# Kernel optimization log

Hardware: AMD Instinct MI355X
Metric: run time of the kernel (lower is better)

## Reference

```python
import jax, jax.numpy as jnp
import numpy as np

N, E, IN_DIM, OUT_DIM, H = 50000, 800000, 128, 16, 8


def setup_inputs() -> dict:
    key = jax.random.key(0)
    ks = jax.random.split(key, 10)
    h = jax.random.normal(ks[0], (N, IN_DIM), dtype=jnp.float32)
    row = jnp.sort(jax.random.randint(ks[1], (E,), 0, N))
    col = jax.random.randint(ks[2], (E,), 0, N)
    s = 1.0 / np.sqrt(IN_DIM)
    Wq = jax.random.normal(ks[3], (IN_DIM, OUT_DIM * H), dtype=jnp.float32) * s
    Wk = jax.random.normal(ks[4], (IN_DIM, OUT_DIM * H), dtype=jnp.float32) * s
    Wv = jax.random.normal(ks[5], (IN_DIM, OUT_DIM * H), dtype=jnp.float32) * s
    bq = jnp.zeros((OUT_DIM * H,), jnp.float32)
    bk = jnp.zeros((OUT_DIM * H,), jnp.float32)
    bv = jnp.zeros((OUT_DIM * H,), jnp.float32)
    return {"h": h, "Wq": Wq, "bq": bq, "Wk": Wk, "bk": bk, "Wv": Wv, "bv": bv,
            "row": row, "col": col}


def reference(h, Wq, bq, Wk, bk, Wv, bv, row, col):
    n = h.shape[0]
    scaling = OUT_DIM ** (-0.5)
    # projections, reshaped (N, out_dim, heads) as in the torch module
    q = (h @ Wq + bq).reshape(n, OUT_DIM, H) * scaling
    k = (h @ Wk + bk).reshape(n, OUT_DIM, H)
    v = (h @ Wv + bv).reshape(n, OUT_DIM, H)
    # bsddmm: per-edge, per-head dot product  score[e,h] = <q[row[e],:,h], k[col[e],:,h]>
    s = jnp.einsum('edh,edh->eh', q[row], k[col])  # [E, H]
    # sparse row-wise softmax (over each destination node's neighbors)
    m = jax.ops.segment_max(s, row, num_segments=n)       # [N, H]
    p = jnp.exp(s - m[row])                               # [E, H]
    z = jax.ops.segment_sum(p, row, num_segments=n)       # [N, H]
    attn = p / z[row]                                     # [E, H]
    # bspmm: out[i,d,h] = sum_{e: row[e]=i} attn[e,h] * v[col[e],d,h]
    out = jax.ops.segment_sum(attn[:, None, :] * v[col], row, num_segments=n)
    return out.reshape(n, -1)
```

## Files before the change

### kernel.cpp

```cpp
#include <hip/hip_runtime.h>
#include <math.h>

typedef unsigned int uint32;
typedef short short8 __attribute__((ext_vector_type(8)));
typedef float f32x4 __attribute__((ext_vector_type(4)));

union frag_u { short8 s; uint32 u[4]; uint4 q; };


__device__ __forceinline__ uint32 pack_bf16(float lo, float hi) {
    uint32 a = __float_as_uint(lo);
    uint32 b = __float_as_uint(hi);
    a = (a + 0x7FFFu + ((a >> 16) & 1u)) >> 16;
    b = (b + 0x7FFFu + ((b >> 16) & 1u)) & 0xFFFF0000u;
    return a | b;
}
__device__ __forceinline__ unsigned short bf16r(float x) {
    uint32 u = __float_as_uint(x);
    return (unsigned short)((u + 0x7FFFu + ((u >> 16) & 1u)) >> 16);
}

__global__ __launch_bounds__(256) void transpose_W_kernel(
    const float* __restrict__ Wq, const float* __restrict__ Wk,
    const float* __restrict__ Wv, uint32* __restrict__ Wt)
{
    __shared__ unsigned short tile[128][129];
    const int m = blockIdx.x;
    const float* W = (m == 0) ? Wq : (m == 1) ? Wk : Wv;
    const int t = threadIdx.x;

    const float4* W4 = reinterpret_cast<const float4*>(W);
    #pragma unroll
    for (int i0 = 0; i0 < 16; ++i0) {
        int i = t + i0 * 256;
        int k = i >> 5, nq = i & 31;
        float4 v = W4[i];
        tile[nq * 4 + 0][k] = bf16r(v.x);
        tile[nq * 4 + 1][k] = bf16r(v.y);
        tile[nq * 4 + 2][k] = bf16r(v.z);
        tile[nq * 4 + 3][k] = bf16r(v.w);
    }
    __syncthreads();
    uint32* out = Wt + (size_t)m * 8192;
    #pragma unroll
    for (int i0 = 0; i0 < 32; ++i0) {
        int i = t + i0 * 256;
        int n = i >> 6, kp = i & 63;
        out[i] = (uint32)tile[n][kp * 2] | ((uint32)tile[n][kp * 2 + 1] << 16);
    }
}

__global__ __launch_bounds__(256) void proj_mfma_kernel(
    const float* __restrict__ h, const uint32* __restrict__ Wt,
    const float* __restrict__ bq, const float* __restrict__ bk,
    const float* __restrict__ bv,
    uint32* __restrict__ Qp, uint2* __restrict__ KV, int N)
{
    const int t = threadIdx.x;
    const int lane = t & 63;
    const int w = t >> 6;
    const int r = lane & 15, g = lane >> 4;
    const int nbase = blockIdx.x * 64;

    frag_u afr[4][4];
    const float4* h4 = reinterpret_cast<const float4*>(h);
    #pragma unroll
    for (int ng = 0; ng < 4; ++ng) {
        int arow = nbase + ng * 16 + r;
        bool av = arow < N;
        #pragma unroll
        for (int kb = 0; kb < 4; ++kb) {
            float4 x = make_float4(0.f,0.f,0.f,0.f), y = x;
            if (av) {
                size_t base = (size_t)arow * 32 + (kb * 4 + g) * 2;
                x = h4[base]; y = h4[base + 1];
            }
            afr[ng][kb].u[0] = pack_bf16(x.x, x.y);
            afr[ng][kb].u[1] = pack_bf16(x.z, x.w);
            afr[ng][kb].u[2] = pack_bf16(y.x, y.y);
            afr[ng][kb].u[3] = pack_bf16(y.z, y.w);
        }
    }

    const float SCALE_Q = 0.25f * 1.44269504f;
    const int c = w * 16 + r;
    uint32 kpk[4][4];

    #pragma unroll
    for (int mat = 0; mat < 3; ++mat) {
        const uint32* wb = Wt + mat * 8192;
        frag_u bfr[2][4];
        #pragma unroll
        for (int tti = 0; tti < 2; ++tti)
            #pragma unroll
            for (int kb = 0; kb < 4; ++kb)
                bfr[tti][kb].q = *reinterpret_cast<const uint4*>(
                    wb + ((w + 4 * tti) * 16 + r) * 64 + (kb * 4 + g) * 4);

        f32x4 acc[4][2];
        #pragma unroll
        for (int ng = 0; ng < 4; ++ng)
            #pragma unroll
            for (int tti = 0; tti < 2; ++tti)
                acc[ng][tti] = (f32x4){0.f, 0.f, 0.f, 0.f};

        #pragma unroll
        for (int ng = 0; ng < 4; ++ng)
            #pragma unroll
            for (int tti = 0; tti < 2; ++tti)
                #pragma unroll
                for (int kb = 0; kb < 4; ++kb)
                    acc[ng][tti] = __builtin_amdgcn_mfma_f32_16x16x32_bf16(
                        afr[ng][kb].s, bfr[tti][kb].s, acc[ng][tti], 0, 0, 0);

        const float* bias = (mat == 0) ? bq : (mat == 1) ? bk : bv;
        float blo = bias[c], bhi = bias[c + 64];
        #pragma unroll
        for (int ng = 0; ng < 4; ++ng) {
            #pragma unroll
            for (int reg = 0; reg < 4; ++reg) {
                int node = nbase + ng * 16 + g * 4 + reg;
                float lo = acc[ng][0][reg] + blo;
                float hi = acc[ng][1][reg] + bhi;
                if (mat == 0) {
                    if (node < N)
                        Qp[(size_t)node * 64 + c] = pack_bf16(lo * SCALE_Q, hi * SCALE_Q);
                } else if (mat == 1) {
                    kpk[ng][reg] = pack_bf16(lo, hi);
                } else {
                    if (node < N)
                        KV[(size_t)node * 64 + c] = make_uint2(kpk[ng][reg], pack_bf16(lo, hi));
                }
            }
        }
    }
}

__global__ void row_ptr_kernel(const int* __restrict__ row, int* __restrict__ rp,
                               int N, int E)
{
    int i = blockIdx.x * blockDim.x + threadIdx.x;
    if (i > N) return;
    int lo = 0, hi = E;
    while (lo < hi) {
        int mid = (lo + hi) >> 1;
        if (row[mid] < i) lo = mid + 1; else hi = mid;
    }
    rp[i] = lo;
}

__global__ __launch_bounds__(256) void edge_attn_kernel(
    const uint32* __restrict__ Qp, const uint2* __restrict__ KV,
    const int* __restrict__ rp, const int* __restrict__ col,
    float* __restrict__ out, int N)
{
    const int lane = threadIdx.x & 63;
    const int node = blockIdx.x * 4 + (threadIdx.x >> 6);
    if (node >= N) return;
    const int hh   = lane & 7;
    const int slot = lane >> 3;

    const int start = rp[node], end = rp[node + 1];
    float* outp = out + (size_t)node * 128;
    if (start >= end) { outp[lane] = 0.f; outp[lane + 64] = 0.f; return; }
    const int last = end - 1;

    float q[16];
    {
        const uint32* qrow = Qp + (size_t)node * 64;
        #pragma unroll
        for (int i = 0; i < 8; ++i) {
            uint32 u = qrow[hh + 8 * i];
            q[2 * i]     = __uint_as_float(u << 16);
            q[2 * i + 1] = __uint_as_float(u & 0xFFFF0000u);
        }
    }

    float z = 0.f;
    float acc[16];
    #pragma unroll
    for (int i = 0; i < 16; ++i) acc[i] = 0.f;

    uint2 bufA[8], bufB[8];
    #define LOADG(buf, c0) { \
        const uint2* kvr = KV + (size_t)(c0) * 64; \
        _Pragma("unroll") \
        for (int i = 0; i < 8; ++i) (buf)[i] = kvr[hh + 8 * i]; }
    #define PROC(buf, gb) { \
        float s = 0.f; \
        _Pragma("unroll") \
        for (int i = 0; i < 8; ++i) { \
            s = fmaf(q[2*i],   __uint_as_float((buf)[i].x << 16), s); \
            s = fmaf(q[2*i+1], __uint_as_float((buf)[i].x & 0xFFFF0000u), s); } \
        float p = ((gb) + slot < end) ? __builtin_amdgcn_exp2f(s) : 0.f; \
        z += p; \
        _Pragma("unroll") \
        for (int i = 0; i < 8; ++i) { \
            acc[i]     = fmaf(p, __uint_as_float((buf)[i].y << 16), acc[i]); \
            acc[8 + i] = fmaf(p, __uint_as_float((buf)[i].y & 0xFFFF0000u), acc[8 + i]); } }

    int cA = col[min(start + slot, last)];
    int cB = col[min(start + 8 + slot, last)];
    LOADG(bufA, cA);
    int gb = start;
    while (true) {
        LOADG(bufB, cB);
        cA = col[min(gb + 16 + slot, last)];
        PROC(bufA, gb);
        gb += 8;
        if (gb >= end) break;
        LOADG(bufA, cA);
        cB = col[min(gb + 16 + slot, last)];
        PROC(bufB, gb);
        gb += 8;
        if (gb >= end) break;
    }

    #pragma unroll
    for (int m = 8; m <= 32; m <<= 1) {
        z += __shfl_xor(z, m);
        #pragma unroll
        for (int i = 0; i < 16; ++i) acc[i] += __shfl_xor(acc[i], m);
    }

    const float rz = 1.0f / z;
    outp[lane]      = acc[slot] * rz;
    outp[lane + 64] = acc[8 + slot] * rz;
}

extern "C" void kernel_launch(void* const* d_in, const int* in_sizes, int n_in,
                              void* d_out, int out_size, void* d_ws, size_t ws_size,
                              hipStream_t stream)
{
    const float* h  = (const float*)d_in[0];
    const float* Wq = (const float*)d_in[1];
    const float* bq = (const float*)d_in[2];
    const float* Wk = (const float*)d_in[3];
    const float* bk = (const float*)d_in[4];
    const float* Wv = (const float*)d_in[5];
    const float* bv = (const float*)d_in[6];
    const int* row  = (const int*)d_in[7];
    const int* col  = (const int*)d_in[8];
    float* out = (float*)d_out;

    const int N = in_sizes[0] / 128;
    const int E = in_sizes[7];

    uint2*  KV = (uint2*)d_ws;
    uint32* Qp = (uint32*)(KV + (size_t)N * 64);
    uint32* Wt = Qp + (size_t)N * 64;
    int*    rp = (int*)(Wt + 3 * 8192);

    transpose_W_kernel<<<3, 256, 0, stream>>>(Wq, Wk, Wv, Wt);
    row_ptr_kernel<<<(N + 256) / 256, 256, 0, stream>>>(row, rp, N, E);
    proj_mfma_kernel<<<(N + 63) / 64, 256, 0, stream>>>(
        h, Wt, bq, bk, bv, Qp, KV, N);
    edge_attn_kernel<<<(N + 3) / 4, 256, 0, stream>>>(Qp, KV, rp, col, out, N);
}
```

Before: 111.0 us.

## Switch intermediates from bf16 to fp16 with packed dot2 and merge prep kernels

Q/K/V and the transposed weights are now stored as fp16, made with the hardware pkrtz convert instead of manual bf16 rounding. The projection uses the f16 MFMA, and the edge kernel computes scores with packed fdot2 instructions in place of unpack-plus-FMA pairs. The weight-transpose and row-pointer kernels are merged into one launch to save launch overhead. Risks are fp16 range limits and round-toward-zero conversion changing accuracy.

```diff
diff --git a/kernel.cpp b/kernel.cpp
--- a/kernel.cpp
+++ b/kernel.cpp
@@ -2,51 +2,65 @@
 #include <math.h>
 
 typedef unsigned int uint32;
-typedef short short8 __attribute__((ext_vector_type(8)));
+typedef _Float16 f16x8 __attribute__((ext_vector_type(8)));
+typedef _Float16 f16x2 __attribute__((ext_vector_type(2)));
 typedef float f32x4 __attribute__((ext_vector_type(4)));
 
-union frag_u { short8 s; uint32 u[4]; uint4 q; };
-
-
-__device__ __forceinline__ uint32 pack_bf16(float lo, float hi) {
-    uint32 a = __float_as_uint(lo);
-    uint32 b = __float_as_uint(hi);
-    a = (a + 0x7FFFu + ((a >> 16) & 1u)) >> 16;
-    b = (b + 0x7FFFu + ((b >> 16) & 1u)) & 0xFFFF0000u;
-    return a | b;
-}
-__device__ __forceinline__ unsigned short bf16r(float x) {
-    uint32 u = __float_as_uint(x);
-    return (unsigned short)((u + 0x7FFFu + ((u >> 16) & 1u)) >> 16);
-}
-
-__global__ __launch_bounds__(256) void transpose_W_kernel(
+union frag_u { f16x8 h; uint32 u[4]; uint4 q; };
+
+
+__device__ __forceinline__ uint32 pack_f16(float lo, float hi) {
+    auto r = __builtin_amdgcn_cvt_pkrtz(lo, hi);
+    return __builtin_bit_cast(uint32, r);
+}
+__device__ __forceinline__ float dot2acc(uint32 a, uint32 b, float c) {
+#if __has_builtin(__builtin_amdgcn_fdot2)
+    return __builtin_amdgcn_fdot2(__builtin_bit_cast(f16x2, a),
+                                  __builtin_bit_cast(f16x2, b), c, false);
+#else
+    f16x2 av = __builtin_bit_cast(f16x2, a), bv = __builtin_bit_cast(f16x2, b);
+    return fmaf((float)av[0], (float)bv[0], fmaf((float)av[1], (float)bv[1], c));
+#endif
+}
+
+__global__ __launch_bounds__(256) void prep_kernel(
     const float* __restrict__ Wq, const float* __restrict__ Wk,
-    const float* __restrict__ Wv, uint32* __restrict__ Wt)
-{
-    __shared__ unsigned short tile[128][129];
-    const int m = blockIdx.x;
-    const float* W = (m == 0) ? Wq : (m == 1) ? Wk : Wv;
+    const float* __restrict__ Wv, uint32* __restrict__ Wt,
+    const int* __restrict__ row, int* __restrict__ rp, int N, int E)
+{
     const int t = threadIdx.x;
-
-    const float4* W4 = reinterpret_cast<const float4*>(W);
-    #pragma unroll
-    for (int i0 = 0; i0 < 16; ++i0) {
-        int i = t + i0 * 256;
-        int k = i >> 5, nq = i & 31;
-        float4 v = W4[i];
-        tile[nq * 4 + 0][k] = bf16r(v.x);
-        tile[nq * 4 + 1][k] = bf16r(v.y);
-        tile[nq * 4 + 2][k] = bf16r(v.z);
-        tile[nq * 4 + 3][k] = bf16r(v.w);
-    }
-    __syncthreads();
-    uint32* out = Wt + (size_t)m * 8192;
-    #pragma unroll
-    for (int i0 = 0; i0 < 32; ++i0) {
-        int i = t + i0 * 256;
-        int n = i >> 6, kp = i & 63;
-        out[i] = (uint32)tile[n][kp * 2] | ((uint32)tile[n][kp * 2 + 1] << 16);
+    if (blockIdx.x < 3) {
+        __shared__ unsigned short tile[128][129];
+        const int m = blockIdx.x;
+        const float* W = (m == 0) ? Wq : (m == 1) ? Wk : Wv;
+        const float4* W4 = reinterpret_cast<const float4*>(W);
+        #pragma unroll
+        for (int i0 = 0; i0 < 16; ++i0) {
+            int i = t + i0 * 256;
+            int k = i >> 5, nq = i & 31;
+            float4 v = W4[i];
+            tile[nq * 4 + 0][k] = (unsigned short)(pack_f16(v.x, 0.f) & 0xFFFFu);
+            tile[nq * 4 + 1][k] = (unsigned short)(pack_f16(v.y, 0.f) & 0xFFFFu);
+            tile[nq * 4 + 2][k] = (unsigned short)(pack_f16(v.z, 0.f) & 0xFFFFu);
+            tile[nq * 4 + 3][k] = (unsigned short)(pack_f16(v.w, 0.f) & 0xFFFFu);
+        }
+        __syncthreads();
+        uint32* out = Wt + (size_t)m * 8192;
+        #pragma unroll
+        for (int i0 = 0; i0 < 32; ++i0) {
+            int i = t + i0 * 256;
+            int n = i >> 6, kp = i & 63;
+            out[i] = (uint32)tile[n][kp * 2] | ((uint32)tile[n][kp * 2 + 1] << 16);
+        }
+    } else {
+        int i = (blockIdx.x - 3) * 256 + t;
+        if (i > N) return;
+        int lo = 0, hi = E;
+        while (lo < hi) {
+            int mid = (lo + hi) >> 1;
+            if (row[mid] < i) lo = mid + 1; else hi = mid;
+        }
+        rp[i] = lo;
     }
 }
 
@@ -75,10 +89,10 @@
                 size_t base = (size_t)arow * 32 + (kb * 4 + g) * 2;
                 x = h4[base]; y = h4[base + 1];
             }
-            afr[ng][kb].u[0] = pack_bf16(x.x, x.y);
-            afr[ng][kb].u[1] = pack_bf16(x.z, x.w);
-            afr[ng][kb].u[2] = pack_bf16(y.x, y.y);
-            afr[ng][kb].u[3] = pack_bf16(y.z, y.w);
+            afr[ng][kb].u[0] = pack_f16(x.x, x.y);
+            afr[ng][kb].u[1] = pack_f16(x.z, x.w);
+            afr[ng][kb].u[2] = pack_f16(y.x, y.y);
+            afr[ng][kb].u[3] = pack_f16(y.z, y.w);
         }
     }
 
@@ -110,8 +124,8 @@
             for (int tti = 0; tti < 2; ++tti)
                 #pragma unroll
                 for (int kb = 0; kb < 4; ++kb)
-                    acc[ng][tti] = __builtin_amdgcn_mfma_f32_16x16x32_bf16(
-                        afr[ng][kb].s, bfr[tti][kb].s, acc[ng][tti], 0, 0, 0);
+                    acc[ng][tti] = __builtin_amdgcn_mfma_f32_16x16x32_f16(
+                        afr[ng][kb].h, bfr[tti][kb].h, acc[ng][tti], 0, 0, 0);
 
         const float* bias = (mat == 0) ? bq : (mat == 1) ? bk : bv;
         float blo = bias[c], bhi = bias[c + 64];
@@ -124,29 +138,16 @@
                 float hi = acc[ng][1][reg] + bhi;
                 if (mat == 0) {
                     if (node < N)
-                        Qp[(size_t)node * 64 + c] = pack_bf16(lo * SCALE_Q, hi * SCALE_Q);
+                        Qp[(size_t)node * 64 + c] = pack_f16(lo * SCALE_Q, hi * SCALE_Q);
                 } else if (mat == 1) {
-                    kpk[ng][reg] = pack_bf16(lo, hi);
+                    kpk[ng][reg] = pack_f16(lo, hi);
                 } else {
                     if (node < N)
-                        KV[(size_t)node * 64 + c] = make_uint2(kpk[ng][reg], pack_bf16(lo, hi));
+                        KV[(size_t)node * 64 + c] = make_uint2(kpk[ng][reg], pack_f16(lo, hi));
                 }
             }
         }
     }
-}
-
-__global__ void row_ptr_kernel(const int* __restrict__ row, int* __restrict__ rp,
-                               int N, int E)
-{
-    int i = blockIdx.x * blockDim.x + threadIdx.x;
-    if (i > N) return;
-    int lo = 0, hi = E;
-    while (lo < hi) {
-        int mid = (lo + hi) >> 1;
-        if (row[mid] < i) lo = mid + 1; else hi = mid;
-    }
-    rp[i] = lo;
 }
 
 __global__ __launch_bounds__(256) void edge_attn_kernel(
@@ -165,15 +166,11 @@
     if (start >= end) { outp[lane] = 0.f; outp[lane + 64] = 0.f; return; }
     const int last = end - 1;
 
-    float q[16];
+    uint32 q[8];
     {
         const uint32* qrow = Qp + (size_t)node * 64;
         #pragma unroll
-        for (int i = 0; i < 8; ++i) {
-            uint32 u = qrow[hh + 8 * i];
-            q[2 * i]     = __uint_as_float(u << 16);
-            q[2 * i + 1] = __uint_as_float(u & 0xFFFF0000u);
-        }
+        for (int i = 0; i < 8; ++i) q[i] = qrow[hh + 8 * i];
     }
 
     float z = 0.f;
@@ -189,15 +186,14 @@
     #define PROC(buf, gb) { \
         float s = 0.f; \
         _Pragma("unroll") \
-        for (int i = 0; i < 8; ++i) { \
-            s = fmaf(q[2*i],   __uint_as_float((buf)[i].x << 16), s); \
-            s = fmaf(q[2*i+1], __uint_as_float((buf)[i].x & 0xFFFF0000u), s); } \
+        for (int i = 0; i < 8; ++i) s = dot2acc(q[i], (buf)[i].x, s); \
         float p = ((gb) + slot < end) ? __builtin_amdgcn_exp2f(s) : 0.f; \
         z += p; \
         _Pragma("unroll") \
         for (int i = 0; i < 8; ++i) { \
-            acc[i]     = fmaf(p, __uint_as_float((buf)[i].y << 16), acc[i]); \
-            acc[8 + i] = fmaf(p, __uint_as_float((buf)[i].y & 0xFFFF0000u), acc[8 + i]); } }
+            f16x2 hv = __builtin_bit_cast(f16x2, (buf)[i].y); \
+            acc[i]     = fmaf(p, (float)hv[0], acc[i]); \
+            acc[8 + i] = fmaf(p, (float)hv[1], acc[8 + i]); } }
 
     int cA = col[min(start + slot, last)];
     int cB = col[min(start + 8 + slot, last)];
@@ -251,8 +247,8 @@
     uint32* Wt = Qp + (size_t)N * 64;
     int*    rp = (int*)(Wt + 3 * 8192);
 
-    transpose_W_kernel<<<3, 256, 0, stream>>>(Wq, Wk, Wv, Wt);
-    row_ptr_kernel<<<(N + 256) / 256, 256, 0, stream>>>(row, rp, N, E);
+    const int rp_blocks = (N + 1 + 255) / 256;
+    prep_kernel<<<3 + rp_blocks, 256, 0, stream>>>(Wq, Wk, Wv, Wt, row, rp, N, E);
     proj_mfma_kernel<<<(N + 63) / 64, 256, 0, stream>>>(
         h, Wt, bq, bk, bv, Qp, KV, N);
     edge_attn_kernel<<<(N + 3) / 4, 256, 0, stream>>>(Qp, KV, rp, col, out, N);
```

Result: faster. 103.8 us (-6.5%).
